# Kernel optimization log

Measured on AMD Instinct MI355X. Metric: run time of the kernel, lower is better.

The kernel has to match this reference:

```python
import jax, jax.numpy as jnp
import numpy as np

B, S, D = 2, 2048, 2048
Q_HEADS, KV_HEADS = 16, 4
D_HEAD = D // Q_HEADS            # 128
GROUPS = Q_HEADS // KV_HEADS     # 4
SCALE = D_HEAD ** -0.5
ROPE_THETA = 10000.0


def apply_rope(x, cos, sin):
    # x: (b, h, s, dh); cos/sin: (s, dh//2) -> rotate interleaved pairs
    xp = x.reshape(*x.shape[:-1], D_HEAD // 2, 2)
    xr, xi = xp[..., 0], xp[..., 1]
    c = cos[None, None, :, :]
    s = sin[None, None, :, :]
    outr = xr * c - xi * s
    outi = xr * s + xi * c
    return jnp.stack([outr, outi], axis=-1).reshape(x.shape)


def setup_inputs() -> dict:
    key = jax.random.key(0)
    ks = jax.random.split(key, 10)
    x = jax.random.normal(ks[0], (B, S, D), dtype=jnp.float32)
    # RoPE angles: pos * inv_freq, shape (S, D_HEAD//2)
    inv_freq = 1.0 / (ROPE_THETA ** (jnp.arange(0, D_HEAD, 2, dtype=jnp.float32) / D_HEAD))
    rope_freq = jnp.arange(S, dtype=jnp.float32)[:, None] * inv_freq[None, :]
    # causal additive mask (1,1,S,S)
    causal = jnp.tril(jnp.ones((S, S), dtype=bool))
    mask = jnp.where(causal, 0.0, -1e9).astype(jnp.float32)[None, None]
    std = D ** -0.5
    wq_w = jax.random.normal(ks[1], (Q_HEADS * D_HEAD, D), dtype=jnp.float32) * std
    wq_b = jnp.zeros((Q_HEADS * D_HEAD,), dtype=jnp.float32)
    wk_w = jax.random.normal(ks[2], (KV_HEADS * D_HEAD, D), dtype=jnp.float32) * std
    wk_b = jnp.zeros((KV_HEADS * D_HEAD,), dtype=jnp.float32)
    wv_w = jax.random.normal(ks[3], (KV_HEADS * D_HEAD, D), dtype=jnp.float32) * std
    wv_b = jnp.zeros((KV_HEADS * D_HEAD,), dtype=jnp.float32)
    wo_w = jax.random.normal(ks[4], (D, Q_HEADS * D_HEAD), dtype=jnp.float32) * std
    wo_b = jnp.zeros((D,), dtype=jnp.float32)
    return {"x": x, "rope_freq": rope_freq, "mask": mask,
            "wq_w": wq_w, "wq_b": wq_b, "wk_w": wk_w, "wk_b": wk_b,
            "wv_w": wv_w, "wv_b": wv_b, "wo_w": wo_w, "wo_b": wo_b}


def reference(x, rope_freq, mask, wq_w, wq_b, wk_w, wk_b, wv_w, wv_b, wo_w, wo_b):
    b, s, d = x.shape
    cos, sin = jnp.cos(rope_freq), jnp.sin(rope_freq)
    # projections (torch Linear: y = x @ W^T + b)
    q = (x @ wq_w.T + wq_b).reshape(b, s, Q_HEADS, D_HEAD).transpose(0, 2, 1, 3)
    k = (x @ wk_w.T + wk_b).reshape(b, s, KV_HEADS, D_HEAD).transpose(0, 2, 1, 3)
    v = (x @ wv_w.T + wv_b).reshape(b, s, KV_HEADS, D_HEAD).transpose(0, 2, 1, 3)
    q = apply_rope(q, cos, sin)
    k = apply_rope(k, cos, sin)
    # GQA: repeat_interleave KV heads to match query heads
    k = jnp.repeat(k, GROUPS, axis=1)  # (b, Q_HEADS, s, dh)
    v = jnp.repeat(v, GROUPS, axis=1)
    scores = jnp.einsum('bhqd,bhkd->bhqk', q, k)
    scores = (scores + mask) * SCALE  # faithful: mask added BEFORE scaling
    attn = jax.nn.softmax(scores, axis=-1)
    out = jnp.einsum('bhqk,bhkd->bhqd', attn, v)
    out = out.transpose(0, 2, 1, 3).reshape(b, s, d)
    return out @ wo_w.T + wo_b
```

## Files before the change

kernel.cpp:

```cpp
#include <hip/hip_runtime.h>
#include <hip/hip_bf16.h>
#include <stdint.h>

typedef float floatx4 __attribute__((ext_vector_type(4)));
typedef __bf16 bfx8 __attribute__((ext_vector_type(8)));

#define ATT_SCALE 0.08838834764831845f

__device__ __forceinline__ uint16_t f2bf(float f) {
  uint32_t u = __float_as_uint(f);
  return (uint16_t)((u + 0x7fffu + ((u >> 16) & 1u)) >> 16);
}
__device__ __forceinline__ float bf2f(uint32_t bits16) {
  return __uint_as_float(bits16 << 16);
}

typedef __attribute__((address_space(3))) uint32_t lds_u32;
typedef const __attribute__((address_space(1))) uint32_t glob_u32;

__device__ __forceinline__ void async_copy16(void* lds, const void* g) {
  uint32_t loff = (uint32_t)(uintptr_t)lds;
  loff = (uint32_t)__builtin_amdgcn_readfirstlane((int)loff);
  lds_u32* lp = reinterpret_cast<lds_u32*>(loff);
  glob_u32* gp = reinterpret_cast<glob_u32*>((uintptr_t)g);
  __builtin_amdgcn_global_load_lds(gp, lp, 16, 0, 0);
}

__global__ void cvt_kernel(const float* __restrict__ in, uint16_t* __restrict__ out, int n) {
  int i = (blockIdx.x * 256 + threadIdx.x) << 2;
  if (i >= n) return;
  const float4 v = *(const float4*)(in + i);
  uint32_t lo = (uint32_t)f2bf(v.x) | ((uint32_t)f2bf(v.y) << 16);
  uint32_t hi = (uint32_t)f2bf(v.z) | ((uint32_t)f2bf(v.w) << 16);
  *(uint2*)(out + i) = make_uint2(lo, hi);
}

__global__ void rope_kernel(uint32_t* __restrict__ buf, const float* __restrict__ freq,
                            int shift, int total) {
  int idx = blockIdx.x * 256 + threadIdx.x;
  if (idx >= total) return;
  int row = idx >> shift;
  int cp  = idx & ((1 << shift) - 1);
  int s = row & 2047;
  int f = cp & 63;
  float fr = freq[(s << 6) + f];
  float sn, c;
  sincosf(fr, &sn, &c);
  uint32_t u = buf[idx];
  float xr = bf2f(u & 0xffffu);
  float xi = bf2f(u >> 16);
  float orr = xr * c - xi * sn;
  float oi  = xr * sn + xi * c;
  buf[idx] = (uint32_t)f2bf(orr) | ((uint32_t)f2bf(oi) << 16);
}

template <int MODE>
__global__ __launch_bounds__(256) void gemm_bt(
    const uint16_t* __restrict__ A,
    const uint16_t* __restrict__ Wq, const uint16_t* __restrict__ Wk,
    const uint16_t* __restrict__ Wv,
    const float* __restrict__ bq, const float* __restrict__ bk,
    const float* __restrict__ bv,
    uint16_t* __restrict__ Qo, uint16_t* __restrict__ Ko,
    uint16_t* __restrict__ Vt, float* __restrict__ Fo) {
  constexpr int Kd = 2048;
  const int tid  = threadIdx.x;
  const int w    = tid >> 6;
  const int lane = tid & 63;
  const int bm = blockIdx.x << 7;
  const int n0 = blockIdx.y << 7;

  const uint16_t* Wp;
  int wrow;
  if (MODE == 0) {
    if (n0 < 2048)      { Wp = Wq; wrow = n0; }
    else if (n0 < 2560) { Wp = Wk; wrow = n0 - 2048; }
    else                { Wp = Wv; wrow = n0 - 2560; }
  } else {
    Wp = Wq; wrow = n0;
  }

  __shared__ uint16_t As[128 * 64];
  __shared__ uint16_t Bs[128 * 64];
  char* AsB = (char*)As;
  char* BsB = (char*)Bs;

  floatx4 acc[4][4] = {};
  const int wr = (w >> 1) << 6;
  const int wc = (w & 1) << 6;

  const int sr  = lane >> 3;
  const int scb = ((lane & 7) ^ sr) << 4;

  const char* Aptr = (const char*)(A + (size_t)(bm + 32 * w + sr) * Kd) + scb;
  const char* Wptr = (const char*)(Wp + (size_t)(wrow + 32 * w + sr) * Kd) + scb;

  for (int k0 = 0; k0 < Kd; k0 += 64) {
#pragma unroll
    for (int i = 0; i < 4; ++i)
      async_copy16(AsB + (32 * w + 8 * i) * 128, Aptr + (size_t)(8 * i) * Kd * 2 + k0 * 2);
#pragma unroll
    for (int i = 0; i < 4; ++i)
      async_copy16(BsB + (32 * w + 8 * i) * 128, Wptr + (size_t)(8 * i) * Kd * 2 + k0 * 2);
    __syncthreads();
#pragma unroll
    for (int kk = 0; kk < 2; ++kk) {
      const int cb = (kk << 6) + ((lane >> 4) << 4);
      bfx8 af[4], bfr[4];
#pragma unroll
      for (int m = 0; m < 4; ++m) {
        int r = wr + (m << 4) + (lane & 15);
        af[m] = *(const bfx8*)(AsB + r * 128 + (cb ^ ((r & 7) << 4)));
      }
#pragma unroll
      for (int n = 0; n < 4; ++n) {
        int r = wc + (n << 4) + (lane & 15);
        bfr[n] = *(const bfx8*)(BsB + r * 128 + (cb ^ ((r & 7) << 4)));
      }
#pragma unroll
      for (int m = 0; m < 4; ++m)
#pragma unroll
        for (int n = 0; n < 4; ++n)
          acc[m][n] = __builtin_amdgcn_mfma_f32_16x16x32_bf16(af[m], bfr[n], acc[m][n], 0, 0, 0);
    }
    __syncthreads();
  }

  const int rb = bm + wr + ((lane >> 4) << 2);
  const int cl = wc + (lane & 15);
#pragma unroll
  for (int n = 0; n < 4; ++n) {
    const int c = n0 + cl + (n << 4);
#pragma unroll
    for (int m = 0; m < 4; ++m) {
      const int r0 = rb + (m << 4);
      if constexpr (MODE == 1) {
        const float bias = bq[c];
#pragma unroll
        for (int j = 0; j < 4; ++j)
          Fo[(size_t)(r0 + j) * 2048 + c] = acc[m][n][j] + bias;
      } else {
        if (n0 < 2048) {
          const float bias = bq[c];
#pragma unroll
          for (int j = 0; j < 4; ++j)
            Qo[(size_t)(r0 + j) * 2048 + c] = f2bf(acc[m][n][j] + bias);
        } else if (n0 < 2560) {
          const int ck = c - 2048;
          const float bias = bk[ck];
#pragma unroll
          for (int j = 0; j < 4; ++j)
            Ko[(size_t)(r0 + j) * 512 + ck] = f2bf(acc[m][n][j] + bias);
        } else {
          const int cv = c - 2560;
          const float bias = bv[cv];
          const int b = r0 >> 11, s = r0 & 2047;
          const int kv = cv >> 7, dh = cv & 127;
          uint32_t lo = (uint32_t)f2bf(acc[m][n][0] + bias) | ((uint32_t)f2bf(acc[m][n][1] + bias) << 16);
          uint32_t hi = (uint32_t)f2bf(acc[m][n][2] + bias) | ((uint32_t)f2bf(acc[m][n][3] + bias) << 16);
          *(uint2*)(Vt + (size_t)(((b << 2) + kv) * 128 + dh) * 2048 + s) = make_uint2(lo, hi);
        }
      }
    }
  }
}

__global__ __launch_bounds__(256) void attn_kernel(
    const uint16_t* __restrict__ Q, const uint16_t* __restrict__ Kb,
    const uint16_t* __restrict__ Vt, uint16_t* __restrict__ O) {
  const int px  = blockIdx.x;
  const int h   = blockIdx.y;
  const int b   = blockIdx.z;
  const int kvh = h >> 2;
  const int tid  = threadIdx.x;
  const int w    = tid >> 6;
  const int lane = tid & 63;
  const int l15 = lane & 15;
  const int l4  = lane >> 4;

  __shared__ uint16_t Ks[2][64 * 128];
  __shared__ uint16_t Vs[2][128 * 64];
  __shared__ uint16_t Ps[4][16 * 64];
  char* PsB = (char*)(Ps[w]);

  const int krow_off = l4;
  const int kscb = l15 << 4;
  const int vrow_off = lane >> 3;
  const int vscb = (lane & 7) << 4;

  auto stageK = [&](int buf, int t) {
    const int kb = t << 6;
#pragma unroll
    for (int i = 0; i < 4; ++i) {
      const int base_r = 16 * w + 4 * i;
      const int r = base_r + krow_off;
      const int scb = kscb ^ ((r & 7) << 4);
      const char* src = (const char*)Kb + ((size_t)(b * 2048 + kb + r) * 512 + kvh * 128) * 2 + scb;
      async_copy16((char*)(Ks[buf]) + base_r * 256, src);
    }
  };
  auto stageV = [&](int buf, int t) {
    const int kb = t << 6;
#pragma unroll
    for (int i = 0; i < 4; ++i) {
      const int base_r = 32 * w + 8 * i;
      const int r = base_r + vrow_off;
      const int scb = vscb ^ ((r & 7) << 4);
      const char* src = (const char*)Vt + ((size_t)(((b << 2) + kvh) * 128 + r) * 2048 + kb) * 2 + scb;
      async_copy16((char*)(Vs[buf]) + base_r * 128, src);
    }
  };

  for (int half = 0; half < 2; ++half) {
    const int qt = half ? (31 - px) : px;
    const int qbase = qt << 6;

    bfx8 qf[4];
    {
      const size_t qrow = (size_t)(b * 2048 + qbase + (w << 4) + l15);
      const char* qp = (const char*)(Q + qrow * 2048 + h * 128 + l4 * 8);
#pragma unroll
      for (int kk = 0; kk < 4; ++kk) qf[kk] = *(const bfx8*)(qp + kk * 64);
    }

    floatx4 oacc[8] = {};
    float mrun[4], lrun[4];
#pragma unroll
    for (int j = 0; j < 4; ++j) { mrun[j] = -1e30f; lrun[j] = 0.0f; }

    stageK(0, 0);
    stageV(0, 0);
    __syncthreads();

    for (int t = 0; t <= qt; ++t) {
      const int cur = t & 1;
      if (t < qt) { stageK(cur ^ 1, t + 1); stageV(cur ^ 1, t + 1); }
      char* KsB = (char*)(Ks[cur]);
      char* VsB = (char*)(Vs[cur]);
      const int kb = t << 6;

      floatx4 sc[4] = {};
      __builtin_amdgcn_s_setprio(1);
#pragma unroll
      for (int kk = 0; kk < 4; ++kk) {
        const int cb = (kk << 6) + (l4 << 4);
#pragma unroll
        for (int n = 0; n < 4; ++n) {
          const int r = (n << 4) + l15;
          bfx8 kf = *(const bfx8*)(KsB + r * 256 + (cb ^ ((r & 7) << 4)));
          sc[n] = __builtin_amdgcn_mfma_f32_16x16x32_bf16(qf[kk], kf, sc[n], 0, 0, 0);
        }
      }
      __builtin_amdgcn_s_setprio(0);

      float p[4][4];
      const bool diag = (t == qt);
#pragma unroll
      for (int n = 0; n < 4; ++n) {
#pragma unroll
        for (int j = 0; j < 4; ++j) {
          float v = sc[n][j] * ATT_SCALE;
          if (diag) {
            const int col = kb + (n << 4) + l15;
            const int row = qbase + (w << 4) + (l4 << 2) + j;
            if (col > row) v = -1e30f;
          }
          p[n][j] = v;
        }
      }

#pragma unroll
      for (int j = 0; j < 4; ++j) {
        float pm = fmaxf(fmaxf(p[0][j], p[1][j]), fmaxf(p[2][j], p[3][j]));
#pragma unroll
        for (int off = 8; off > 0; off >>= 1) pm = fmaxf(pm, __shfl_xor(pm, off, 64));
        const float mnew = fmaxf(mrun[j], pm);
        const float sf = __expf(mrun[j] - mnew);
        mrun[j] = mnew;
        float rs = 0.f;
#pragma unroll
        for (int n = 0; n < 4; ++n) {
          p[n][j] = __expf(p[n][j] - mnew);
          rs += p[n][j];
        }
        lrun[j] = lrun[j] * sf + rs;
#pragma unroll
        for (int d = 0; d < 8; ++d) oacc[d][j] *= sf;
      }

#pragma unroll
      for (int n = 0; n < 4; ++n) {
        const int cbw = (n << 5) + (l15 << 1);
#pragma unroll
        for (int j = 0; j < 4; ++j) {
          const int r = (l4 << 2) + j;
          *(uint16_t*)(PsB + r * 128 + (cbw ^ ((r & 7) << 4))) = f2bf(p[n][j]);
        }
      }

      __builtin_amdgcn_s_setprio(1);
#pragma unroll
      for (int kk = 0; kk < 2; ++kk) {
        const int cb = (kk << 6) + (l4 << 4);
        bfx8 pf = *(const bfx8*)(PsB + l15 * 128 + (cb ^ ((l15 & 7) << 4)));
#pragma unroll
        for (int d = 0; d < 8; ++d) {
          const int r = (d << 4) + l15;
          bfx8 vf = *(const bfx8*)(VsB + r * 128 + (cb ^ ((r & 7) << 4)));
          oacc[d] = __builtin_amdgcn_mfma_f32_16x16x32_bf16(pf, vf, oacc[d], 0, 0, 0);
        }
      }
      __builtin_amdgcn_s_setprio(0);

      __syncthreads();
    }

#pragma unroll
    for (int j = 0; j < 4; ++j) {
      float l = lrun[j];
#pragma unroll
      for (int off = 8; off > 0; off >>= 1) l += __shfl_xor(l, off, 64);
      const float inv = 1.0f / l;
      const size_t row = (size_t)(b * 2048 + qbase + (w << 4) + (l4 << 2) + j);
#pragma unroll
      for (int d = 0; d < 8; ++d) {
        const int c = h * 128 + (d << 4) + l15;
        O[row * 2048 + c] = f2bf(oacc[d][j] * inv);
      }
    }
  }
}

extern "C" void kernel_launch(void* const* d_in, const int* in_sizes, int n_in,
                              void* d_out, int out_size, void* d_ws, size_t ws_size,
                              hipStream_t stream) {
  (void)in_sizes; (void)n_in; (void)out_size; (void)ws_size;
  const float* x         = (const float*)d_in[0];
  const float* rope_freq = (const float*)d_in[1];
  const float* wq_w = (const float*)d_in[3];
  const float* wq_b = (const float*)d_in[4];
  const float* wk_w = (const float*)d_in[5];
  const float* wk_b = (const float*)d_in[6];
  const float* wv_w = (const float*)d_in[7];
  const float* wv_b = (const float*)d_in[8];
  const float* wo_w = (const float*)d_in[9];
  const float* wo_b = (const float*)d_in[10];
  float* out = (float*)d_out;

  char* ws = (char*)d_ws;
  uint16_t* xbf = (uint16_t*)(ws + 0);
  uint16_t* wqb = (uint16_t*)(ws + 16777216);
  uint16_t* wkb = (uint16_t*)(ws + 25165824);
  uint16_t* wvb = (uint16_t*)(ws + 27262976);
  uint16_t* wob = (uint16_t*)(ws + 29360128);
  uint16_t* qbf = (uint16_t*)(ws + 37748736);
  uint16_t* kbf = (uint16_t*)(ws + 54525952);
  uint16_t* vtb = (uint16_t*)(ws + 58720256);
  uint16_t* att = (uint16_t*)(ws + 62914560);

  cvt_kernel<<<8192, 256, 0, stream>>>(x, xbf, 8388608);
  cvt_kernel<<<4096, 256, 0, stream>>>(wq_w, wqb, 4194304);
  cvt_kernel<<<1024, 256, 0, stream>>>(wk_w, wkb, 1048576);
  cvt_kernel<<<1024, 256, 0, stream>>>(wv_w, wvb, 1048576);
  cvt_kernel<<<4096, 256, 0, stream>>>(wo_w, wob, 4194304);

  gemm_bt<0><<<dim3(32, 24), 256, 0, stream>>>(xbf, wqb, wkb, wvb, wq_b, wk_b, wv_b,
                                               qbf, kbf, vtb, nullptr);

  rope_kernel<<<16384, 256, 0, stream>>>((uint32_t*)qbf, rope_freq, 10, 4194304);
  rope_kernel<<<4096, 256, 0, stream>>>((uint32_t*)kbf, rope_freq, 8, 1048576);

  attn_kernel<<<dim3(16, 16, 2), 256, 0, stream>>>(qbf, kbf, vtb, att);

  gemm_bt<1><<<dim3(32, 16), 256, 0, stream>>>(att, wob, nullptr, nullptr, wo_b, nullptr,
                                               nullptr, nullptr, nullptr, nullptr, out);
}
```

Measured before the change: 368.0 us.

## Use double-buffered 256-wide GEMM tiles, fold softmax scale into Q RoPE, skip rescale

Replaces the 128x128 single-buffered projection GEMMs with 512-thread kernels using 256-column tiles and two LDS stages, so async global-to-LDS loads for the next K tiles overlap the MFMA work on the current one. The attention scale is applied to Q during RoPE instead of per score element. The online softmax now skips the accumulator rescale when no lane's running max increases. These add register and LDS pressure and give fewer workgroups, and folding the scale before bf16 rounding slightly changes numerics.

Measured after the change: 455.6 us. 23.8% more time.

```diff
diff --git a/kernel.cpp b/kernel.cpp
--- a/kernel.cpp
+++ b/kernel.cpp
@@ -36,7 +36,7 @@
 }
 
 __global__ void rope_kernel(uint32_t* __restrict__ buf, const float* __restrict__ freq,
-                            int shift, int total) {
+                            int shift, int total, float post) {
   int idx = blockIdx.x * 256 + threadIdx.x;
   if (idx >= total) return;
   int row = idx >> shift;
@@ -49,13 +49,13 @@
   uint32_t u = buf[idx];
   float xr = bf2f(u & 0xffffu);
   float xi = bf2f(u >> 16);
-  float orr = xr * c - xi * sn;
-  float oi  = xr * sn + xi * c;
+  float orr = (xr * c - xi * sn) * post;
+  float oi  = (xr * sn + xi * c) * post;
   buf[idx] = (uint32_t)f2bf(orr) | ((uint32_t)f2bf(oi) << 16);
 }
 
-template <int MODE>
-__global__ __launch_bounds__(256) void gemm_bt(
+template <int BM, int WGM, int MODE>
+__global__ __launch_bounds__(512, 2) void gemm256(
     const uint16_t* __restrict__ A,
     const uint16_t* __restrict__ Wq, const uint16_t* __restrict__ Wk,
     const uint16_t* __restrict__ Wv,
@@ -63,16 +63,25 @@
     const float* __restrict__ bv,
     uint16_t* __restrict__ Qo, uint16_t* __restrict__ Ko,
     uint16_t* __restrict__ Vt, float* __restrict__ Fo) {
-  constexpr int Kd = 2048;
+  constexpr int BN = 256;
+  constexpr int NT = 32;
+  constexpr int WGN = 8 / WGM;
+  constexpr int WN = BN / WGN;
+  constexpr int NR = WN / 16;
+  constexpr int AI = BM / 64;
+  constexpr int NL = AI + 4;
+
   const int tid  = threadIdx.x;
   const int w    = tid >> 6;
   const int lane = tid & 63;
-  const int bm = blockIdx.x << 7;
-  const int n0 = blockIdx.y << 7;
+  const int l15  = lane & 15;
+  const int l4   = lane >> 4;
+  const int bm = blockIdx.x * BM;
+  const int n0 = blockIdx.y * BN;
 
   const uint16_t* Wp;
   int wrow;
-  if (MODE == 0) {
+  if constexpr (MODE == 0) {
     if (n0 < 2048)      { Wp = Wq; wrow = n0; }
     else if (n0 < 2560) { Wp = Wk; wrow = n0 - 2048; }
     else                { Wp = Wv; wrow = n0 - 2560; }
@@ -80,59 +89,105 @@
     Wp = Wq; wrow = n0;
   }
 
-  __shared__ uint16_t As[128 * 64];
-  __shared__ uint16_t Bs[128 * 64];
-  char* AsB = (char*)As;
-  char* BsB = (char*)Bs;
-
-  floatx4 acc[4][4] = {};
-  const int wr = (w >> 1) << 6;
-  const int wc = (w & 1) << 6;
-
-  const int sr  = lane >> 3;
-  const int scb = ((lane & 7) ^ sr) << 4;
-
-  const char* Aptr = (const char*)(A + (size_t)(bm + 32 * w + sr) * Kd) + scb;
-  const char* Wptr = (const char*)(Wp + (size_t)(wrow + 32 * w + sr) * Kd) + scb;
-
-  for (int k0 = 0; k0 < Kd; k0 += 64) {
-#pragma unroll
-    for (int i = 0; i < 4; ++i)
-      async_copy16(AsB + (32 * w + 8 * i) * 128, Aptr + (size_t)(8 * i) * Kd * 2 + k0 * 2);
-#pragma unroll
-    for (int i = 0; i < 4; ++i)
-      async_copy16(BsB + (32 * w + 8 * i) * 128, Wptr + (size_t)(8 * i) * Kd * 2 + k0 * 2);
-    __syncthreads();
-#pragma unroll
-    for (int kk = 0; kk < 2; ++kk) {
-      const int cb = (kk << 6) + ((lane >> 4) << 4);
-      bfx8 af[4], bfr[4];
-#pragma unroll
-      for (int m = 0; m < 4; ++m) {
-        int r = wr + (m << 4) + (lane & 15);
-        af[m] = *(const bfx8*)(AsB + r * 128 + (cb ^ ((r & 7) << 4)));
-      }
-#pragma unroll
-      for (int n = 0; n < 4; ++n) {
-        int r = wc + (n << 4) + (lane & 15);
-        bfr[n] = *(const bfx8*)(BsB + r * 128 + (cb ^ ((r & 7) << 4)));
-      }
-#pragma unroll
-      for (int m = 0; m < 4; ++m)
-#pragma unroll
-        for (int n = 0; n < 4; ++n)
-          acc[m][n] = __builtin_amdgcn_mfma_f32_16x16x32_bf16(af[m], bfr[n], acc[m][n], 0, 0, 0);
-    }
-    __syncthreads();
+  __shared__ uint16_t As[2][BM * 64];
+  __shared__ uint16_t Bs[2][BN * 64];
+
+  const int wr = w / WGN;
+  const int wc = w % WGN;
+
+  floatx4 acc[8][NR] = {};
+
+  const int srow = lane >> 3;
+  const int sx   = lane & 7;
+
+  auto stageA = [&](int buf, int t) {
+#pragma unroll
+    for (int i = 0; i < AI; ++i) {
+      const int base_r = w * (BM / 8) + 8 * i;
+      const int r = base_r + srow;
+      const char* src = (const char*)A + ((size_t)(bm + r) * 2048 + t * 64) * 2 + ((sx ^ (r & 7)) << 4);
+      async_copy16((char*)(As[buf]) + base_r * 128, src);
+    }
+  };
+  auto stageB = [&](int buf, int t) {
+#pragma unroll
+    for (int i = 0; i < 4; ++i) {
+      const int base_r = w * 32 + 8 * i;
+      const int r = base_r + srow;
+      const char* src = (const char*)Wp + ((size_t)(wrow + r) * 2048 + t * 64) * 2 + ((sx ^ (r & 7)) << 4);
+      async_copy16((char*)(Bs[buf]) + base_r * 128, src);
+    }
+  };
+
+  stageA(0, 0); stageB(0, 0);
+  stageA(1, 1); stageB(1, 1);
+  if constexpr (NL == 8) asm volatile("s_waitcnt vmcnt(8)" ::: "memory");
+  else                   asm volatile("s_waitcnt vmcnt(6)" ::: "memory");
+  __builtin_amdgcn_s_barrier();
+
+  for (int t = 0; t < NT; ++t) {
+    const int cur = t & 1;
+    const char* AsB = (const char*)(As[cur]);
+    const char* BsB = (const char*)(Bs[cur]);
+
+    bfx8 a0[8], b0[NR];
+#pragma unroll
+    for (int n = 0; n < NR; ++n) {
+      const int r = wc * WN + n * 16 + l15;
+      b0[n] = *(const bfx8*)(BsB + r * 128 + ((l4 << 4) ^ ((r & 7) << 4)));
+    }
+#pragma unroll
+    for (int m = 0; m < 8; ++m) {
+      const int r = wr * 128 + m * 16 + l15;
+      a0[m] = *(const bfx8*)(AsB + r * 128 + ((l4 << 4) ^ ((r & 7) << 4)));
+    }
+    __builtin_amdgcn_s_setprio(1);
+#pragma unroll
+    for (int m = 0; m < 8; ++m)
+#pragma unroll
+      for (int n = 0; n < NR; ++n)
+        acc[m][n] = __builtin_amdgcn_mfma_f32_16x16x32_bf16(a0[m], b0[n], acc[m][n], 0, 0, 0);
+    __builtin_amdgcn_s_setprio(0);
+
+    bfx8 a1[8], b1[NR];
+#pragma unroll
+    for (int n = 0; n < NR; ++n) {
+      const int r = wc * WN + n * 16 + l15;
+      b1[n] = *(const bfx8*)(BsB + r * 128 + ((64 + (l4 << 4)) ^ ((r & 7) << 4)));
+    }
+#pragma unroll
+    for (int m = 0; m < 8; ++m) {
+      const int r = wr * 128 + m * 16 + l15;
+      a1[m] = *(const bfx8*)(AsB + r * 128 + ((64 + (l4 << 4)) ^ ((r & 7) << 4)));
+    }
+    asm volatile("s_waitcnt lgkmcnt(0)" ::: "memory");
+    __builtin_amdgcn_sched_barrier(0);
+    __builtin_amdgcn_s_barrier();
+    if (t + 2 < NT) { stageA(cur, t + 2); stageB(cur, t + 2); }
+    __builtin_amdgcn_sched_barrier(0);
+    __builtin_amdgcn_s_setprio(1);
+#pragma unroll
+    for (int m = 0; m < 8; ++m)
+#pragma unroll
+      for (int n = 0; n < NR; ++n)
+        acc[m][n] = __builtin_amdgcn_mfma_f32_16x16x32_bf16(a1[m], b1[n], acc[m][n], 0, 0, 0);
+    __builtin_amdgcn_s_setprio(0);
+    if (t < NT - 2) {
+      if constexpr (NL == 8) asm volatile("s_waitcnt vmcnt(8)" ::: "memory");
+      else                   asm volatile("s_waitcnt vmcnt(6)" ::: "memory");
+    } else if (t == NT - 2) {
+      asm volatile("s_waitcnt vmcnt(0)" ::: "memory");
+    }
+    __builtin_amdgcn_s_barrier();
   }
 
-  const int rb = bm + wr + ((lane >> 4) << 2);
-  const int cl = wc + (lane & 15);
-#pragma unroll
-  for (int n = 0; n < 4; ++n) {
+  const int rb = bm + wr * 128 + (l4 << 2);
+  const int cl = wc * WN + l15;
+#pragma unroll
+  for (int n = 0; n < NR; ++n) {
     const int c = n0 + cl + (n << 4);
 #pragma unroll
-    for (int m = 0; m < 4; ++m) {
+    for (int m = 0; m < 8; ++m) {
       const int r0 = rb + (m << 4);
       if constexpr (MODE == 1) {
         const float bias = bq[c];
@@ -259,7 +314,7 @@
       for (int n = 0; n < 4; ++n) {
 #pragma unroll
         for (int j = 0; j < 4; ++j) {
-          float v = sc[n][j] * ATT_SCALE;
+          float v = sc[n][j];
           if (diag) {
             const int col = kb + (n << 4) + l15;
             const int row = qbase + (w << 4) + (l4 << 2) + j;
@@ -274,18 +329,28 @@
         float pm = fmaxf(fmaxf(p[0][j], p[1][j]), fmaxf(p[2][j], p[3][j]));
 #pragma unroll
         for (int off = 8; off > 0; off >>= 1) pm = fmaxf(pm, __shfl_xor(pm, off, 64));
-        const float mnew = fmaxf(mrun[j], pm);
-        const float sf = __expf(mrun[j] - mnew);
-        mrun[j] = mnew;
-        float rs = 0.f;
-#pragma unroll
-        for (int n = 0; n < 4; ++n) {
-          p[n][j] = __expf(p[n][j] - mnew);
-          rs += p[n][j];
-        }
-        lrun[j] = lrun[j] * sf + rs;
-#pragma unroll
-        for (int d = 0; d < 8; ++d) oacc[d][j] *= sf;
+        if (__any(pm > mrun[j])) {
+          const float mnew = fmaxf(mrun[j], pm);
+          const float sf = __expf(mrun[j] - mnew);
+          mrun[j] = mnew;
+          float rs = 0.f;
+#pragma unroll
+          for (int n = 0; n < 4; ++n) {
+            p[n][j] = __expf(p[n][j] - mnew);
+            rs += p[n][j];
+          }
+          lrun[j] = lrun[j] * sf + rs;
+#pragma unroll
+          for (int d = 0; d < 8; ++d) oacc[d][j] *= sf;
+        } else {
+          float rs = 0.f;
+#pragma unroll
+          for (int n = 0; n < 4; ++n) {
+            p[n][j] = __expf(p[n][j] - mrun[j]);
+            rs += p[n][j];
+          }
+          lrun[j] += rs;
+        }
       }
 
 #pragma unroll
@@ -364,14 +429,15 @@
   cvt_kernel<<<1024, 256, 0, stream>>>(wv_w, wvb, 1048576);
   cvt_kernel<<<4096, 256, 0, stream>>>(wo_w, wob, 4194304);
 
-  gemm_bt<0><<<dim3(32, 24), 256, 0, stream>>>(xbf, wqb, wkb, wvb, wq_b, wk_b, wv_b,
-                                               qbf, kbf, vtb, nullptr);
-
-  rope_kernel<<<16384, 256, 0, stream>>>((uint32_t*)qbf, rope_freq, 10, 4194304);
-  rope_kernel<<<4096, 256, 0, stream>>>((uint32_t*)kbf, rope_freq, 8, 1048576);
+  gemm256<256, 2, 0><<<dim3(16, 12), 512, 0, stream>>>(
+      xbf, wqb, wkb, wvb, wq_b, wk_b, wv_b, qbf, kbf, vtb, nullptr);
+
+  rope_kernel<<<16384, 256, 0, stream>>>((uint32_t*)qbf, rope_freq, 10, 4194304, ATT_SCALE);
+  rope_kernel<<<4096, 256, 0, stream>>>((uint32_t*)kbf, rope_freq, 8, 1048576, 1.0f);
 
   attn_kernel<<<dim3(16, 16, 2), 256, 0, stream>>>(qbf, kbf, vtb, att);
 
-  gemm_bt<1><<<dim3(32, 16), 256, 0, stream>>>(att, wob, nullptr, nullptr, wo_b, nullptr,
-                                               nullptr, nullptr, nullptr, nullptr, out);
-}
+  gemm256<128, 1, 1><<<dim3(32, 8), 512, 0, stream>>>(
+      att, wob, nullptr, nullptr, wo_b, nullptr, nullptr,
+      nullptr, nullptr, nullptr, out);
+}
```

## Pipeline GEMMs with triple-buffered LDS, merge conversion/rope launches, fold scale into Q

Applied to the files above, without the earlier changes.

Replaces the single-buffered GEMM with a 512-thread, 256-wide-N kernel that uses a three-stage async global-to-LDS pipeline and a single barrier per K step. The five conversion launches and the two rope launches are each merged into one launch. The attention scale is folded into Q during rope, which removes a multiply from the attention inner loop. These changes target launch overhead and memory-latency stalls in the projection GEMMs, at the cost of more LDS per block and fewer blocks in the grid.

Result: faster. 335.7 us (-8.8%).

```diff
diff --git a/kernel.cpp b/kernel.cpp
--- a/kernel.cpp
+++ b/kernel.cpp
@@ -26,36 +26,49 @@
   __builtin_amdgcn_global_load_lds(gp, lp, 16, 0, 0);
 }
 
-__global__ void cvt_kernel(const float* __restrict__ in, uint16_t* __restrict__ out, int n) {
-  int i = (blockIdx.x * 256 + threadIdx.x) << 2;
-  if (i >= n) return;
-  const float4 v = *(const float4*)(in + i);
+__global__ void cvt5_kernel(const float* __restrict__ x,  const float* __restrict__ wq,
+                            const float* __restrict__ wk, const float* __restrict__ wv,
+                            const float* __restrict__ wo,
+                            uint16_t* __restrict__ xb,  uint16_t* __restrict__ wqb,
+                            uint16_t* __restrict__ wkb, uint16_t* __restrict__ wvb,
+                            uint16_t* __restrict__ wob) {
+  const int bid = blockIdx.x;
+  const float* src; uint16_t* dst; int base;
+  if (bid < 8192)       { src = x;  dst = xb;  base = 0; }
+  else if (bid < 12288) { src = wq; dst = wqb; base = 8192; }
+  else if (bid < 13312) { src = wk; dst = wkb; base = 12288; }
+  else if (bid < 14336) { src = wv; dst = wvb; base = 13312; }
+  else                  { src = wo; dst = wob; base = 14336; }
+  const int i = (((bid - base) << 8) + threadIdx.x) << 2;
+  const float4 v = *(const float4*)(src + i);
   uint32_t lo = (uint32_t)f2bf(v.x) | ((uint32_t)f2bf(v.y) << 16);
   uint32_t hi = (uint32_t)f2bf(v.z) | ((uint32_t)f2bf(v.w) << 16);
-  *(uint2*)(out + i) = make_uint2(lo, hi);
-}
-
-__global__ void rope_kernel(uint32_t* __restrict__ buf, const float* __restrict__ freq,
-                            int shift, int total) {
-  int idx = blockIdx.x * 256 + threadIdx.x;
-  if (idx >= total) return;
-  int row = idx >> shift;
-  int cp  = idx & ((1 << shift) - 1);
-  int s = row & 2047;
-  int f = cp & 63;
-  float fr = freq[(s << 6) + f];
+  *(uint2*)(dst + i) = make_uint2(lo, hi);
+}
+
+__global__ void rope2_kernel(uint32_t* __restrict__ qb, uint32_t* __restrict__ kb,
+                             const float* __restrict__ freq) {
+  const int bid = blockIdx.x;
+  uint32_t* buf; int idx, shift; float post;
+  if (bid < 16384) { buf = qb; idx = (bid << 8) + threadIdx.x; shift = 10; post = ATT_SCALE; }
+  else { buf = kb; idx = ((bid - 16384) << 8) + threadIdx.x; shift = 8; post = 1.0f; }
+  const int row = idx >> shift;
+  const int cp  = idx & ((1 << shift) - 1);
+  const int s = row & 2047;
+  const int f = cp & 63;
+  const float fr = freq[(s << 6) + f];
   float sn, c;
   sincosf(fr, &sn, &c);
-  uint32_t u = buf[idx];
-  float xr = bf2f(u & 0xffffu);
-  float xi = bf2f(u >> 16);
-  float orr = xr * c - xi * sn;
-  float oi  = xr * sn + xi * c;
+  const uint32_t u = buf[idx];
+  const float xr = bf2f(u & 0xffffu);
+  const float xi = bf2f(u >> 16);
+  const float orr = (xr * c - xi * sn) * post;
+  const float oi  = (xr * sn + xi * c) * post;
   buf[idx] = (uint32_t)f2bf(orr) | ((uint32_t)f2bf(oi) << 16);
 }
 
-template <int MODE>
-__global__ __launch_bounds__(256) void gemm_bt(
+template <int BM, int MODE>
+__global__ __launch_bounds__(512, 2) void gemm3(
     const uint16_t* __restrict__ A,
     const uint16_t* __restrict__ Wq, const uint16_t* __restrict__ Wk,
     const uint16_t* __restrict__ Wv,
@@ -63,16 +76,23 @@
     const float* __restrict__ bv,
     uint16_t* __restrict__ Qo, uint16_t* __restrict__ Ko,
     uint16_t* __restrict__ Vt, float* __restrict__ Fo) {
-  constexpr int Kd = 2048;
+  constexpr int NT  = 64;
+  constexpr int MR  = BM / 32;
+  constexpr int NLW = BM / 128 + 2;
+
   const int tid  = threadIdx.x;
   const int w    = tid >> 6;
   const int lane = tid & 63;
-  const int bm = blockIdx.x << 7;
-  const int n0 = blockIdx.y << 7;
+  const int l15  = lane & 15;
+  const int l4   = lane >> 4;
+  const int wr   = w >> 2;
+  const int wc   = w & 3;
+  const int bm = blockIdx.x * BM;
+  const int n0 = blockIdx.y * 256;
 
   const uint16_t* Wp;
   int wrow;
-  if (MODE == 0) {
+  if constexpr (MODE == 0) {
     if (n0 < 2048)      { Wp = Wq; wrow = n0; }
     else if (n0 < 2560) { Wp = Wk; wrow = n0 - 2048; }
     else                { Wp = Wv; wrow = n0 - 2560; }
@@ -80,59 +100,83 @@
     Wp = Wq; wrow = n0;
   }
 
-  __shared__ uint16_t As[128 * 64];
-  __shared__ uint16_t Bs[128 * 64];
-  char* AsB = (char*)As;
-  char* BsB = (char*)Bs;
-
-  floatx4 acc[4][4] = {};
-  const int wr = (w >> 1) << 6;
-  const int wc = (w & 1) << 6;
-
-  const int sr  = lane >> 3;
-  const int scb = ((lane & 7) ^ sr) << 4;
-
-  const char* Aptr = (const char*)(A + (size_t)(bm + 32 * w + sr) * Kd) + scb;
-  const char* Wptr = (const char*)(Wp + (size_t)(wrow + 32 * w + sr) * Kd) + scb;
-
-  for (int k0 = 0; k0 < Kd; k0 += 64) {
-#pragma unroll
-    for (int i = 0; i < 4; ++i)
-      async_copy16(AsB + (32 * w + 8 * i) * 128, Aptr + (size_t)(8 * i) * Kd * 2 + k0 * 2);
-#pragma unroll
-    for (int i = 0; i < 4; ++i)
-      async_copy16(BsB + (32 * w + 8 * i) * 128, Wptr + (size_t)(8 * i) * Kd * 2 + k0 * 2);
-    __syncthreads();
-#pragma unroll
-    for (int kk = 0; kk < 2; ++kk) {
-      const int cb = (kk << 6) + ((lane >> 4) << 4);
-      bfx8 af[4], bfr[4];
-#pragma unroll
-      for (int m = 0; m < 4; ++m) {
-        int r = wr + (m << 4) + (lane & 15);
-        af[m] = *(const bfx8*)(AsB + r * 128 + (cb ^ ((r & 7) << 4)));
-      }
-#pragma unroll
-      for (int n = 0; n < 4; ++n) {
-        int r = wc + (n << 4) + (lane & 15);
-        bfr[n] = *(const bfx8*)(BsB + r * 128 + (cb ^ ((r & 7) << 4)));
-      }
-#pragma unroll
-      for (int m = 0; m < 4; ++m)
-#pragma unroll
-        for (int n = 0; n < 4; ++n)
-          acc[m][n] = __builtin_amdgcn_mfma_f32_16x16x32_bf16(af[m], bfr[n], acc[m][n], 0, 0, 0);
-    }
-    __syncthreads();
+  __shared__ uint16_t As[3][BM * 32];
+  __shared__ uint16_t Bs[3][256 * 32];
+
+  floatx4 acc[MR][4] = {};
+
+  const int srow = lane >> 2;
+  const int sg   = lane & 3;
+
+  auto stageA = [&](int buf, int t) {
+#pragma unroll
+    for (int i = 0; i < BM / 128; ++i) {
+      const int r0i = w * (BM / 8) + i * 16;
+      const int r = r0i + srow;
+      const char* src = (const char*)A +
+          ((size_t)(bm + r) * 2048 + t * 32) * 2 + ((sg ^ (r & 3)) << 4);
+      async_copy16((char*)(As[buf]) + r0i * 64, src);
+    }
+  };
+  auto stageB = [&](int buf, int t) {
+#pragma unroll
+    for (int i = 0; i < 2; ++i) {
+      const int r0i = w * 32 + i * 16;
+      const int r = r0i + srow;
+      const char* src = (const char*)Wp +
+          ((size_t)(wrow + r) * 2048 + t * 32) * 2 + ((sg ^ (r & 3)) << 4);
+      async_copy16((char*)(Bs[buf]) + r0i * 64, src);
+    }
+  };
+
+  stageA(0, 0); stageB(0, 0);
+  stageA(1, 1); stageB(1, 1);
+  asm volatile("s_waitcnt vmcnt(%0)" :: "i"(NLW) : "memory");
+  __builtin_amdgcn_s_barrier();
+
+  int c0 = 0;
+  for (int t = 0; t < NT; ++t) {
+    const char* AsB = (const char*)(As[c0]);
+    const char* BsB = (const char*)(Bs[c0]);
+
+    bfx8 bf_[4], af_[MR];
+#pragma unroll
+    for (int n = 0; n < 4; ++n) {
+      const int r = wc * 64 + n * 16 + l15;
+      bf_[n] = *(const bfx8*)(BsB + r * 64 + ((l4 ^ (r & 3)) << 4));
+    }
+#pragma unroll
+    for (int m = 0; m < MR; ++m) {
+      const int r = wr * (BM / 2) + m * 16 + l15;
+      af_[m] = *(const bfx8*)(AsB + r * 64 + ((l4 ^ (r & 3)) << 4));
+    }
+
+    int c2 = c0 + 2; if (c2 >= 3) c2 -= 3;
+    if (t + 2 < NT) { stageA(c2, t + 2); stageB(c2, t + 2); }
+
+    asm volatile("s_waitcnt lgkmcnt(0)" ::: "memory");
+    __builtin_amdgcn_sched_barrier(0);
+    __builtin_amdgcn_s_setprio(1);
+#pragma unroll
+    for (int m = 0; m < MR; ++m)
+#pragma unroll
+      for (int n = 0; n < 4; ++n)
+        acc[m][n] = __builtin_amdgcn_mfma_f32_16x16x32_bf16(af_[m], bf_[n], acc[m][n], 0, 0, 0);
+    __builtin_amdgcn_s_setprio(0);
+
+    if (t + 2 < NT)      asm volatile("s_waitcnt vmcnt(%0)" :: "i"(NLW) : "memory");
+    else if (t + 1 < NT) asm volatile("s_waitcnt vmcnt(0)" ::: "memory");
+    if (t + 1 < NT) __builtin_amdgcn_s_barrier();
+    if (++c0 == 3) c0 = 0;
   }
 
-  const int rb = bm + wr + ((lane >> 4) << 2);
-  const int cl = wc + (lane & 15);
+  const int rb = bm + wr * (BM / 2) + (l4 << 2);
+  const int cl = wc * 64 + l15;
 #pragma unroll
   for (int n = 0; n < 4; ++n) {
     const int c = n0 + cl + (n << 4);
 #pragma unroll
-    for (int m = 0; m < 4; ++m) {
+    for (int m = 0; m < MR; ++m) {
       const int r0 = rb + (m << 4);
       if constexpr (MODE == 1) {
         const float bias = bq[c];
@@ -259,7 +303,7 @@
       for (int n = 0; n < 4; ++n) {
 #pragma unroll
         for (int j = 0; j < 4; ++j) {
-          float v = sc[n][j] * ATT_SCALE;
+          float v = sc[n][j];
           if (diag) {
             const int col = kb + (n << 4) + l15;
             const int row = qbase + (w << 4) + (l4 << 2) + j;
@@ -358,20 +402,17 @@
   uint16_t* vtb = (uint16_t*)(ws + 58720256);
   uint16_t* att = (uint16_t*)(ws + 62914560);
 
-  cvt_kernel<<<8192, 256, 0, stream>>>(x, xbf, 8388608);
-  cvt_kernel<<<4096, 256, 0, stream>>>(wq_w, wqb, 4194304);
-  cvt_kernel<<<1024, 256, 0, stream>>>(wk_w, wkb, 1048576);
-  cvt_kernel<<<1024, 256, 0, stream>>>(wv_w, wvb, 1048576);
-  cvt_kernel<<<4096, 256, 0, stream>>>(wo_w, wob, 4194304);
-
-  gemm_bt<0><<<dim3(32, 24), 256, 0, stream>>>(xbf, wqb, wkb, wvb, wq_b, wk_b, wv_b,
-                                               qbf, kbf, vtb, nullptr);
-
-  rope_kernel<<<16384, 256, 0, stream>>>((uint32_t*)qbf, rope_freq, 10, 4194304);
-  rope_kernel<<<4096, 256, 0, stream>>>((uint32_t*)kbf, rope_freq, 8, 1048576);
+  cvt5_kernel<<<18432, 256, 0, stream>>>(x, wq_w, wk_w, wv_w, wo_w,
+                                         xbf, wqb, wkb, wvb, wob);
+
+  gemm3<256, 0><<<dim3(16, 12), 512, 0, stream>>>(
+      xbf, wqb, wkb, wvb, wq_b, wk_b, wv_b, qbf, kbf, vtb, nullptr);
+
+  rope2_kernel<<<20480, 256, 0, stream>>>((uint32_t*)qbf, (uint32_t*)kbf, rope_freq);
 
   attn_kernel<<<dim3(16, 16, 2), 256, 0, stream>>>(qbf, kbf, vtb, att);
 
-  gemm_bt<1><<<dim3(32, 16), 256, 0, stream>>>(att, wob, nullptr, nullptr, wo_b, nullptr,
-                                               nullptr, nullptr, nullptr, nullptr, out);
-}
+  gemm3<128, 1><<<dim3(32, 8), 512, 0, stream>>>(
+      att, wob, nullptr, nullptr, wo_b, nullptr, nullptr,
+      nullptr, nullptr, nullptr, out);
+}
```
